# Performance work log

Measured on AMD Instinct MI355X. Metric: run time of the kernel, lower is better.

The kernel has to match this reference:

```python
import jax, jax.numpy as jnp
import numpy as np

N, E, F_IN, NHID, HEADS, NGRAPHS = 50000, 800000, 128, 256, 4, 16
C = NHID // HEADS          # 64 per-head channels
NEG_SLOPE = 0.2            # PyG GATConv default negative_slope


def setup_inputs() -> dict:
    key = jax.random.key(0)
    k = jax.random.split(key, 7)
    x = jax.random.normal(k[0], (N, F_IN), jnp.float32)
    edge_index = jax.random.randint(k[1], (2, E), 0, N)          # [2, E] src/dst
    batch = jnp.sort(jax.random.randint(k[2], (N,), 0, NGRAPHS))  # node -> graph id
    # learned params of GATConv(F_IN, C, heads=HEADS), concat=True
    W = jax.random.normal(k[3], (F_IN, NHID), jnp.float32) / np.sqrt(F_IN)
    att_src = jax.random.normal(k[4], (HEADS, C), jnp.float32) * 0.1
    att_dst = jax.random.normal(k[5], (HEADS, C), jnp.float32) * 0.1
    bias = jax.random.normal(k[6], (NHID,), jnp.float32) * 0.01
    return {"x": x, "edge_index": edge_index, "batch": batch,
            "W": W, "att_src": att_src, "att_dst": att_dst, "bias": bias}


def _segment_softmax(logits, seg, num_segments):
    # softmax over all edges sharing the same destination node
    m = jax.ops.segment_max(logits, seg, num_segments=num_segments)
    m = jnp.where(jnp.isfinite(m), m, jnp.zeros_like(m))  # guard empty segments
    e = jnp.exp(logits - m[seg])
    s = jax.ops.segment_sum(e, seg, num_segments=num_segments)
    return e / (s[seg] + 1e-16)


def reference(x, edge_index, batch, W, att_src, att_dst, bias):
    n = x.shape[0]
    # PyG GATConv adds self-loops by default
    loops = jnp.arange(n, dtype=edge_index.dtype)
    src = jnp.concatenate([edge_index[0], loops])
    dst = jnp.concatenate([edge_index[1], loops])
    xp = (x @ W).reshape(n, HEADS, C)                       # [N, H, C]
    a_src = jnp.einsum('nhc,hc->nh', xp, att_src)           # [N, H]
    a_dst = jnp.einsum('nhc,hc->nh', xp, att_dst)
    logits = jax.nn.leaky_relu(a_src[src] + a_dst[dst], NEG_SLOPE)  # [E+N, H]
    alpha = _segment_softmax(logits, dst, n)
    msg = xp[src] * alpha[:, :, None]                       # [E+N, H, C]
    out = jax.ops.segment_sum(msg, dst, num_segments=n).reshape(n, NHID) + bias
    h = jax.nn.relu(out)                                    # hidden_act='relu'
    # global max / mean pooling per graph, then concat
    gmax = jax.ops.segment_max(h, batch, num_segments=NGRAPHS)
    cnt = jax.ops.segment_sum(jnp.ones((n, 1), h.dtype), batch, num_segments=NGRAPHS)
    gmean = jax.ops.segment_sum(h, batch, num_segments=NGRAPHS) / (cnt + 1e-16)
    return jnp.concatenate([gmax, gmean], axis=1)           # [NGRAPHS, 2*NHID]
```

## Files before the change

### kernel.cpp

```cpp
#include <hip/hip_runtime.h>

#define NN 50000
#define NE 800000
#define FIN 128
#define NHID 256
#define HEADS 4
#define CPH 64
#define NG 16
#define ETOT (NE + NN)
#define NEG_SLOPE 0.2f
#define MAXDEG 64

__device__ __forceinline__ float lrelu(float x) {
    return x > 0.f ? x : NEG_SLOPE * x;
}
__device__ __forceinline__ unsigned short bf16_rne(float f) {
    unsigned u = __float_as_uint(f);
    unsigned r = (u + 0x7fffu + ((u >> 16) & 1u)) >> 16;
    return (unsigned short)r;
}
__device__ __forceinline__ float bf16_to_f(unsigned short h) {
    return __uint_as_float((unsigned)h << 16);
}

__global__ __launch_bounds__(256) void k_gemm(const float* __restrict__ x,
                                              const float* __restrict__ W,
                                              const float* __restrict__ att_src,
                                              const float* __restrict__ att_dst,
                                              unsigned short* __restrict__ xp16,
                                              float* __restrict__ a_src,
                                              float* __restrict__ a_dst) {
    __shared__ float xs[32][33];
    __shared__ float ws[32][256];
    const int tid = threadIdx.x;
    const int row0 = blockIdx.x * 32;
    const int cc = tid & 31;
    const int tc = cc * 4;
    const int tr = (tid >> 5) * 4;
    float acc[4][8] = {};

    for (int k0 = 0; k0 < FIN; k0 += 32) {
        {
            int r = tid >> 3;
            int c = (tid & 7) << 2;
            int gr = row0 + r;
            float4 v = make_float4(0.f, 0.f, 0.f, 0.f);
            if (gr < NN) v = *(const float4*)&x[(size_t)gr * FIN + k0 + c];
            xs[r][c] = v.x; xs[r][c + 1] = v.y; xs[r][c + 2] = v.z; xs[r][c + 3] = v.w;
        }
        {
            int c4 = (tid & 63) * 4;
            int rbase = (tid >> 6) * 8;
            #pragma unroll
            for (int i = 0; i < 8; i++) {
                float4 v = *(const float4*)&W[(size_t)(k0 + rbase + i) * NHID + c4];
                *(float4*)&ws[rbase + i][c4] = v;
            }
        }
        __syncthreads();
        #pragma unroll
        for (int k = 0; k < 32; k++) {
            float4 b1 = *(const float4*)&ws[k][tc];
            float4 b2 = *(const float4*)&ws[k][tc + 128];
            #pragma unroll
            for (int i = 0; i < 4; i++) {
                float a = xs[tr + i][k];
                acc[i][0] += a * b1.x; acc[i][1] += a * b1.y;
                acc[i][2] += a * b1.z; acc[i][3] += a * b1.w;
                acc[i][4] += a * b2.x; acc[i][5] += a * b2.y;
                acc[i][6] += a * b2.z; acc[i][7] += a * b2.w;
            }
        }
        __syncthreads();
    }

    float4 as1 = *(const float4*)&att_src[tc];
    float4 as2 = *(const float4*)&att_src[tc + 128];
    float4 ad1 = *(const float4*)&att_dst[tc];
    float4 ad2 = *(const float4*)&att_dst[tc + 128];
    int h1 = cc >> 4;
    #pragma unroll
    for (int i = 0; i < 4; i++) {
        int row = row0 + tr + i;
        bool rowok = row < NN;
        if (rowok) {
            ushort4 o1, o2;
            o1.x = bf16_rne(acc[i][0]); o1.y = bf16_rne(acc[i][1]);
            o1.z = bf16_rne(acc[i][2]); o1.w = bf16_rne(acc[i][3]);
            o2.x = bf16_rne(acc[i][4]); o2.y = bf16_rne(acc[i][5]);
            o2.z = bf16_rne(acc[i][6]); o2.w = bf16_rne(acc[i][7]);
            *(ushort4*)&xp16[(size_t)row * NHID + tc] = o1;
            *(ushort4*)&xp16[(size_t)row * NHID + tc + 128] = o2;
        }
        float p1s = acc[i][0] * as1.x + acc[i][1] * as1.y + acc[i][2] * as1.z + acc[i][3] * as1.w;
        float p2s = acc[i][4] * as2.x + acc[i][5] * as2.y + acc[i][6] * as2.z + acc[i][7] * as2.w;
        float p1d = acc[i][0] * ad1.x + acc[i][1] * ad1.y + acc[i][2] * ad1.z + acc[i][3] * ad1.w;
        float p2d = acc[i][4] * ad2.x + acc[i][5] * ad2.y + acc[i][6] * ad2.z + acc[i][7] * ad2.w;
        #pragma unroll
        for (int off = 1; off < 16; off <<= 1) {
            p1s += __shfl_xor(p1s, off, 64);
            p2s += __shfl_xor(p2s, off, 64);
            p1d += __shfl_xor(p1d, off, 64);
            p2d += __shfl_xor(p2d, off, 64);
        }
        if ((tid & 15) == 0 && rowok) {
            a_src[row * 4 + h1]     = p1s;
            a_src[row * 4 + h1 + 2] = p2s;
            a_dst[row * 4 + h1]     = p1d;
            a_dst[row * 4 + h1 + 2] = p2d;
        }
    }
}

__global__ __launch_bounds__(256) void k_scatter(const int* __restrict__ ei,
                                                 int* __restrict__ deg,
                                                 unsigned short* __restrict__ elist) {
    int e = blockIdx.x * 256 + threadIdx.x;
    if (e >= ETOT) return;
    int s, d;
    if (e < NE) { s = ei[e]; d = ei[NE + e]; } else { s = d = e - NE; }
    int pos = atomicAdd(&deg[d], 1);
    if (pos < MAXDEG) elist[d * MAXDEG + pos] = (unsigned short)s;
}

__global__ __launch_bounds__(256) void k_agg(const unsigned short* __restrict__ elist,
                                             const int* __restrict__ deg,
                                             const float* __restrict__ a_src,
                                             const float* __restrict__ a_dst,
                                             const unsigned short* __restrict__ xp16,
                                             const float* __restrict__ bias,
                                             float* __restrict__ hbuf) {
    __shared__ float wlds[4][MAXDEG][4];
    __shared__ int   slds[4][MAXDEG];
    int wv = threadIdx.x >> 6;
    int lane = threadIdx.x & 63;
    int d = blockIdx.x * 4 + wv;
    if (d >= NN) return;
    int dg = deg[d]; if (dg > MAXDEG) dg = MAXDEG;

    float4 ad = *(const float4*)&a_dst[d * 4];

    float4 lg = make_float4(-1e30f, -1e30f, -1e30f, -1e30f);
    if (lane < dg) {
        int s = elist[d * MAXDEG + lane];
        slds[wv][lane] = s;
        float4 as = *(const float4*)&a_src[s * 4];
        lg.x = lrelu(as.x + ad.x);
        lg.y = lrelu(as.y + ad.y);
        lg.z = lrelu(as.z + ad.z);
        lg.w = lrelu(as.w + ad.w);
    }
    float4 m = lg;
    #pragma unroll
    for (int off = 1; off < 64; off <<= 1) {
        m.x = fmaxf(m.x, __shfl_xor(m.x, off, 64));
        m.y = fmaxf(m.y, __shfl_xor(m.y, off, 64));
        m.z = fmaxf(m.z, __shfl_xor(m.z, off, 64));
        m.w = fmaxf(m.w, __shfl_xor(m.w, off, 64));
    }
    float4 w = make_float4(0.f, 0.f, 0.f, 0.f);
    if (lane < dg) {
        w.x = expf(lg.x - m.x);
        w.y = expf(lg.y - m.y);
        w.z = expf(lg.z - m.z);
        w.w = expf(lg.w - m.w);
    }
    *(float4*)&wlds[wv][lane][0] = w;
    float4 sm = w;
    #pragma unroll
    for (int off = 1; off < 64; off <<= 1) {
        sm.x += __shfl_xor(sm.x, off, 64);
        sm.y += __shfl_xor(sm.y, off, 64);
        sm.z += __shfl_xor(sm.z, off, 64);
        sm.w += __shfl_xor(sm.w, off, 64);
    }
    int h = lane >> 4;
    float denom = (h == 0 ? sm.x : h == 1 ? sm.y : h == 2 ? sm.z : sm.w) + 1e-16f;

    float4 acc = make_float4(0.f, 0.f, 0.f, 0.f);
    for (int e = 0; e < dg; e++) {
        int s = slds[wv][e];
        float we = wlds[wv][e][h];
        ushort4 v = *(const ushort4*)&xp16[(size_t)s * NHID + lane * 4];
        acc.x += we * bf16_to_f(v.x);
        acc.y += we * bf16_to_f(v.y);
        acc.z += we * bf16_to_f(v.z);
        acc.w += we * bf16_to_f(v.w);
    }
    float4 b = *(const float4*)&bias[lane * 4];
    float4 hv;
    hv.x = fmaxf(acc.x / denom + b.x, 0.f);
    hv.y = fmaxf(acc.y / denom + b.y, 0.f);
    hv.z = fmaxf(acc.z / denom + b.z, 0.f);
    hv.w = fmaxf(acc.w / denom + b.w, 0.f);
    *(float4*)&hbuf[(size_t)d * NHID + lane * 4] = hv;
}

#define NPB 128
__global__ __launch_bounds__(256) void k_pool(const float* __restrict__ hbuf,
                                              const int* __restrict__ batch,
                                              float* __restrict__ gmax,
                                              float* __restrict__ gsum) {
    int c = threadIdx.x;
    int n0 = blockIdx.x * NPB;
    if (n0 >= NN) return;
    float lmax = 0.f, lsum = 0.f;
    int cur_g = batch[n0];
    int nend = n0 + NPB; if (nend > NN) nend = NN;
    for (int n = n0; n < nend; n++) {
        int g = batch[n];
        if (g != cur_g) {
            atomicMax((int*)&gmax[cur_g * NHID + c], __float_as_int(lmax));
            atomicAdd(&gsum[cur_g * NHID + c], lsum);
            lmax = 0.f; lsum = 0.f; cur_g = g;
        }
        float val = hbuf[(size_t)n * NHID + c];
        lmax = fmaxf(lmax, val);
        lsum += val;
    }
    atomicMax((int*)&gmax[cur_g * NHID + c], __float_as_int(lmax));
    atomicAdd(&gsum[cur_g * NHID + c], lsum);
}

__device__ __forceinline__ int lb_batch(const int* __restrict__ batch, int val) {
    int lo = 0, hi = NN;
    while (lo < hi) {
        int mid = (lo + hi) >> 1;
        if (batch[mid] < val) lo = mid + 1; else hi = mid;
    }
    return lo;
}

__global__ __launch_bounds__(512) void k_final(const float* __restrict__ gmax,
                                               const float* __restrict__ gsum,
                                               const int* __restrict__ batch,
                                               float* __restrict__ out) {
    __shared__ float inv_cnt;
    int g = blockIdx.x;
    if (threadIdx.x == 0) {
        int lo = lb_batch(batch, g);
        int hi = lb_batch(batch, g + 1);
        inv_cnt = 1.0f / ((float)(hi - lo) + 1e-16f);
    }
    __syncthreads();
    int j = threadIdx.x;
    float v;
    if (j < 256) v = gmax[g * NHID + j];
    else v = gsum[g * NHID + (j - 256)] * inv_cnt;
    out[g * 512 + j] = v;
}

extern "C" void kernel_launch(void* const* d_in, const int* in_sizes, int n_in,
                              void* d_out, int out_size, void* d_ws, size_t ws_size,
                              hipStream_t stream) {
    const float* x      = (const float*)d_in[0];
    const int*   ei     = (const int*)d_in[1];
    const int*   batch  = (const int*)d_in[2];
    const float* W      = (const float*)d_in[3];
    const float* attS   = (const float*)d_in[4];
    const float* attD   = (const float*)d_in[5];
    const float* bias   = (const float*)d_in[6];
    float* out = (float*)d_out;

    float* ws = (float*)d_ws;
    unsigned short* xp16  = (unsigned short*)ws;
    float*          a_src = (float*)(xp16 + (size_t)NN * NHID + 256);
    float*          a_dst = a_src + 200000;
    float*          hbuf  = a_dst + 200000;
    unsigned short* elist = (unsigned short*)(hbuf + 12800000);
    int*            deg   = (int*)(elist + (size_t)NN * MAXDEG);
    float*          gmax  = (float*)(deg + NN);
    float*          gsum  = gmax + 4096;

    size_t zero_bytes = (size_t)(NN + 4096 + 4096) * 4;
    hipMemsetAsync((void*)deg, 0, zero_bytes, stream);

    k_gemm<<<(NN + 31) / 32, 256, 0, stream>>>(x, W, attS, attD, xp16, a_src, a_dst);
    k_scatter<<<(ETOT + 255) / 256, 256, 0, stream>>>(ei, deg, elist);
    k_agg<<<(NN + 3) / 4, 256, 0, stream>>>(elist, deg, a_src, a_dst, xp16, bias, hbuf);
    k_pool<<<(NN + NPB - 1) / NPB, 256, 0, stream>>>(hbuf, batch, gmax, gsum);
    k_final<<<NG, 512, 0, stream>>>(gmax, gsum, batch, out);
}
```

Before: 299.2 us.

## Use bf16 MFMA for projection GEMM and unroll aggregation gather loop

```diff
diff --git a/kernel.cpp b/kernel.cpp
--- a/kernel.cpp
+++ b/kernel.cpp
@@ -23,91 +23,118 @@
     return __uint_as_float((unsigned)h << 16);
 }
 
+using frag_ab = __attribute__((ext_vector_type(8))) short;
+using frag_cd = __attribute__((ext_vector_type(4))) float;
+
+__global__ __launch_bounds__(256) void k_prep(const float* __restrict__ W,
+                                              unsigned short* __restrict__ Wt16) {
+    int idx = blockIdx.x * 256 + threadIdx.x;
+    int n = idx >> 7;
+    int k = idx & 127;
+    Wt16[idx] = bf16_rne(W[(size_t)k * NHID + n]);
+}
+
 __global__ __launch_bounds__(256) void k_gemm(const float* __restrict__ x,
-                                              const float* __restrict__ W,
+                                              const unsigned short* __restrict__ Wt16,
                                               const float* __restrict__ att_src,
                                               const float* __restrict__ att_dst,
                                               unsigned short* __restrict__ xp16,
                                               float* __restrict__ a_src,
                                               float* __restrict__ a_dst) {
-    __shared__ float xs[32][33];
-    __shared__ float ws[32][256];
+    __shared__ __align__(16) unsigned short xs[64][136];
     const int tid = threadIdx.x;
-    const int row0 = blockIdx.x * 32;
-    const int cc = tid & 31;
-    const int tc = cc * 4;
-    const int tr = (tid >> 5) * 4;
-    float acc[4][8] = {};
-
-    for (int k0 = 0; k0 < FIN; k0 += 32) {
-        {
-            int r = tid >> 3;
-            int c = (tid & 7) << 2;
-            int gr = row0 + r;
-            float4 v = make_float4(0.f, 0.f, 0.f, 0.f);
-            if (gr < NN) v = *(const float4*)&x[(size_t)gr * FIN + k0 + c];
-            xs[r][c] = v.x; xs[r][c + 1] = v.y; xs[r][c + 2] = v.z; xs[r][c + 3] = v.w;
-        }
-        {
-            int c4 = (tid & 63) * 4;
-            int rbase = (tid >> 6) * 8;
+    const int row0 = blockIdx.x * 64;
+
+    {
+        int r = tid >> 2;
+        int c0 = (tid & 3) * 32;
+        int gr = row0 + r;
+        if (gr < NN) {
             #pragma unroll
             for (int i = 0; i < 8; i++) {
-                float4 v = *(const float4*)&W[(size_t)(k0 + rbase + i) * NHID + c4];
-                *(float4*)&ws[rbase + i][c4] = v;
-            }
+                float4 v = *(const float4*)&x[(size_t)gr * FIN + c0 + i * 4];
+                ushort4 o;
+                o.x = bf16_rne(v.x); o.y = bf16_rne(v.y);
+                o.z = bf16_rne(v.z); o.w = bf16_rne(v.w);
+                *(ushort4*)&xs[r][c0 + i * 4] = o;
+            }
+        } else {
+            ushort4 z = {0, 0, 0, 0};
+            #pragma unroll
+            for (int i = 0; i < 8; i++) *(ushort4*)&xs[r][c0 + i * 4] = z;
         }
-        __syncthreads();
+    }
+    __syncthreads();
+
+    const int wv = tid >> 6;
+    const int lane = tid & 63;
+    const int rowhalf = wv >> 1;
+    const int colhalf = wv & 1;
+    const int m = lane & 15;
+    const int q = lane >> 4;
+    const int cbase = colhalf * 128;
+
+    frag_cd acc[2][8];
+    #pragma unroll
+    for (int rt = 0; rt < 2; rt++)
         #pragma unroll
-        for (int k = 0; k < 32; k++) {
-            float4 b1 = *(const float4*)&ws[k][tc];
-            float4 b2 = *(const float4*)&ws[k][tc + 128];
+        for (int c = 0; c < 8; c++)
+            acc[rt][c] = (frag_cd){0.f, 0.f, 0.f, 0.f};
+
+    #pragma unroll
+    for (int k0 = 0; k0 < FIN; k0 += 32) {
+        frag_ab af0 = *(const frag_ab*)&xs[rowhalf * 32 + m][k0 + q * 8];
+        frag_ab af1 = *(const frag_ab*)&xs[rowhalf * 32 + 16 + m][k0 + q * 8];
+        #pragma unroll
+        for (int c = 0; c < 8; c++) {
+            int n = cbase + c * 16 + m;
+            frag_ab bf = *(const frag_ab*)&Wt16[(size_t)n * FIN + k0 + q * 8];
+            acc[0][c] = __builtin_amdgcn_mfma_f32_16x16x32_bf16(af0, bf, acc[0][c], 0, 0, 0);
+            acc[1][c] = __builtin_amdgcn_mfma_f32_16x16x32_bf16(af1, bf, acc[1][c], 0, 0, 0);
+        }
+    }
+
+    float asv[8], adv[8];
+    #pragma unroll
+    for (int c = 0; c < 8; c++) {
+        asv[c] = att_src[cbase + c * 16 + m];
+        adv[c] = att_dst[cbase + c * 16 + m];
+    }
+    const int headA = colhalf * 2;
+    const int headB = colhalf * 2 + 1;
+
+    #pragma unroll
+    for (int rt = 0; rt < 2; rt++) {
+        #pragma unroll
+        for (int reg = 0; reg < 4; reg++) {
+            int grow = row0 + rowhalf * 32 + rt * 16 + q * 4 + reg;
+            bool ok = grow < NN;
+            if (ok) {
+                #pragma unroll
+                for (int c = 0; c < 8; c++)
+                    xp16[(size_t)grow * NHID + cbase + c * 16 + m] = bf16_rne(acc[rt][c][reg]);
+            }
+            float psA = 0.f, psB = 0.f, pdA = 0.f, pdB = 0.f;
             #pragma unroll
-            for (int i = 0; i < 4; i++) {
-                float a = xs[tr + i][k];
-                acc[i][0] += a * b1.x; acc[i][1] += a * b1.y;
-                acc[i][2] += a * b1.z; acc[i][3] += a * b1.w;
-                acc[i][4] += a * b2.x; acc[i][5] += a * b2.y;
-                acc[i][6] += a * b2.z; acc[i][7] += a * b2.w;
-            }
-        }
-        __syncthreads();
-    }
-
-    float4 as1 = *(const float4*)&att_src[tc];
-    float4 as2 = *(const float4*)&att_src[tc + 128];
-    float4 ad1 = *(const float4*)&att_dst[tc];
-    float4 ad2 = *(const float4*)&att_dst[tc + 128];
-    int h1 = cc >> 4;
-    #pragma unroll
-    for (int i = 0; i < 4; i++) {
-        int row = row0 + tr + i;
-        bool rowok = row < NN;
-        if (rowok) {
-            ushort4 o1, o2;
-            o1.x = bf16_rne(acc[i][0]); o1.y = bf16_rne(acc[i][1]);
-            o1.z = bf16_rne(acc[i][2]); o1.w = bf16_rne(acc[i][3]);
-            o2.x = bf16_rne(acc[i][4]); o2.y = bf16_rne(acc[i][5]);
-            o2.z = bf16_rne(acc[i][6]); o2.w = bf16_rne(acc[i][7]);
-            *(ushort4*)&xp16[(size_t)row * NHID + tc] = o1;
-            *(ushort4*)&xp16[(size_t)row * NHID + tc + 128] = o2;
-        }
-        float p1s = acc[i][0] * as1.x + acc[i][1] * as1.y + acc[i][2] * as1.z + acc[i][3] * as1.w;
-        float p2s = acc[i][4] * as2.x + acc[i][5] * as2.y + acc[i][6] * as2.z + acc[i][7] * as2.w;
-        float p1d = acc[i][0] * ad1.x + acc[i][1] * ad1.y + acc[i][2] * ad1.z + acc[i][3] * ad1.w;
-        float p2d = acc[i][4] * ad2.x + acc[i][5] * ad2.y + acc[i][6] * ad2.z + acc[i][7] * ad2.w;
-        #pragma unroll
-        for (int off = 1; off < 16; off <<= 1) {
-            p1s += __shfl_xor(p1s, off, 64);
-            p2s += __shfl_xor(p2s, off, 64);
-            p1d += __shfl_xor(p1d, off, 64);
-            p2d += __shfl_xor(p2d, off, 64);
-        }
-        if ((tid & 15) == 0 && rowok) {
-            a_src[row * 4 + h1]     = p1s;
-            a_src[row * 4 + h1 + 2] = p2s;
-            a_dst[row * 4 + h1]     = p1d;
-            a_dst[row * 4 + h1 + 2] = p2d;
+            for (int c = 0; c < 4; c++) {
+                psA += acc[rt][c][reg] * asv[c];
+                pdA += acc[rt][c][reg] * adv[c];
+                psB += acc[rt][c + 4][reg] * asv[c + 4];
+                pdB += acc[rt][c + 4][reg] * adv[c + 4];
+            }
+            #pragma unroll
+            for (int off = 1; off < 16; off <<= 1) {
+                psA += __shfl_xor(psA, off, 64);
+                psB += __shfl_xor(psB, off, 64);
+                pdA += __shfl_xor(pdA, off, 64);
+                pdB += __shfl_xor(pdB, off, 64);
+            }
+            if (m == 0 && ok) {
+                a_src[grow * 4 + headA] = psA;
+                a_src[grow * 4 + headB] = psB;
+                a_dst[grow * 4 + headA] = pdA;
+                a_dst[grow * 4 + headB] = pdB;
+            }
         }
     }
 }
@@ -177,16 +204,42 @@
     int h = lane >> 4;
     float denom = (h == 0 ? sm.x : h == 1 ? sm.y : h == 2 ? sm.z : sm.w) + 1e-16f;
 
-    float4 acc = make_float4(0.f, 0.f, 0.f, 0.f);
-    for (int e = 0; e < dg; e++) {
-        int s = slds[wv][e];
-        float we = wlds[wv][e][h];
-        ushort4 v = *(const ushort4*)&xp16[(size_t)s * NHID + lane * 4];
-        acc.x += we * bf16_to_f(v.x);
-        acc.y += we * bf16_to_f(v.y);
-        acc.z += we * bf16_to_f(v.z);
-        acc.w += we * bf16_to_f(v.w);
-    }
+    float4 acc0 = make_float4(0.f, 0.f, 0.f, 0.f);
+    float4 acc1 = make_float4(0.f, 0.f, 0.f, 0.f);
+    float4 acc2 = make_float4(0.f, 0.f, 0.f, 0.f);
+    float4 acc3 = make_float4(0.f, 0.f, 0.f, 0.f);
+    int e = 0;
+    for (; e + 4 <= dg; e += 4) {
+        int s0 = slds[wv][e + 0], s1 = slds[wv][e + 1];
+        int s2 = slds[wv][e + 2], s3 = slds[wv][e + 3];
+        float w0 = wlds[wv][e + 0][h], w1 = wlds[wv][e + 1][h];
+        float w2 = wlds[wv][e + 2][h], w3 = wlds[wv][e + 3][h];
+        ushort4 v0 = *(const ushort4*)&xp16[(size_t)s0 * NHID + lane * 4];
+        ushort4 v1 = *(const ushort4*)&xp16[(size_t)s1 * NHID + lane * 4];
+        ushort4 v2 = *(const ushort4*)&xp16[(size_t)s2 * NHID + lane * 4];
+        ushort4 v3 = *(const ushort4*)&xp16[(size_t)s3 * NHID + lane * 4];
+        acc0.x += w0 * bf16_to_f(v0.x); acc0.y += w0 * bf16_to_f(v0.y);
+        acc0.z += w0 * bf16_to_f(v0.z); acc0.w += w0 * bf16_to_f(v0.w);
+        acc1.x += w1 * bf16_to_f(v1.x); acc1.y += w1 * bf16_to_f(v1.y);
+        acc1.z += w1 * bf16_to_f(v1.z); acc1.w += w1 * bf16_to_f(v1.w);
+        acc2.x += w2 * bf16_to_f(v2.x); acc2.y += w2 * bf16_to_f(v2.y);
+        acc2.z += w2 * bf16_to_f(v2.z); acc2.w += w2 * bf16_to_f(v2.w);
+        acc3.x += w3 * bf16_to_f(v3.x); acc3.y += w3 * bf16_to_f(v3.y);
+        acc3.z += w3 * bf16_to_f(v3.z); acc3.w += w3 * bf16_to_f(v3.w);
+    }
+    for (; e < dg; e++) {
+        int s0 = slds[wv][e];
+        float w0 = wlds[wv][e][h];
+        ushort4 v0 = *(const ushort4*)&xp16[(size_t)s0 * NHID + lane * 4];
+        acc0.x += w0 * bf16_to_f(v0.x); acc0.y += w0 * bf16_to_f(v0.y);
+        acc0.z += w0 * bf16_to_f(v0.z); acc0.w += w0 * bf16_to_f(v0.w);
+    }
+    float4 acc;
+    acc.x = (acc0.x + acc1.x) + (acc2.x + acc3.x);
+    acc.y = (acc0.y + acc1.y) + (acc2.y + acc3.y);
+    acc.z = (acc0.z + acc1.z) + (acc2.z + acc3.z);
+    acc.w = (acc0.w + acc1.w) + (acc2.w + acc3.w);
+
     float4 b = *(const float4*)&bias[lane * 4];
     float4 hv;
     hv.x = fmaxf(acc.x / denom + b.x, 0.f);
@@ -271,11 +324,13 @@
     int*            deg   = (int*)(elist + (size_t)NN * MAXDEG);
     float*          gmax  = (float*)(deg + NN);
     float*          gsum  = gmax + 4096;
+    unsigned short* Wt16  = (unsigned short*)(gsum + 4096);
 
     size_t zero_bytes = (size_t)(NN + 4096 + 4096) * 4;
     hipMemsetAsync((void*)deg, 0, zero_bytes, stream);
 
-    k_gemm<<<(NN + 31) / 32, 256, 0, stream>>>(x, W, attS, attD, xp16, a_src, a_dst);
+    k_prep<<<128, 256, 0, stream>>>(W, Wt16);
+    k_gemm<<<(NN + 63) / 64, 256, 0, stream>>>(x, Wt16, attS, attD, xp16, a_src, a_dst);
     k_scatter<<<(ETOT + 255) / 256, 256, 0, stream>>>(ei, deg, elist);
     k_agg<<<(NN + 3) / 4, 256, 0, stream>>>(elist, deg, a_src, a_dst, xp16, bias, hbuf);
     k_pool<<<(NN + NPB - 1) / NPB, 256, 0, stream>>>(hbuf, batch, gmax, gsum);
```

After: 275.1 us. 1.09x faster.
